# Kernel optimization log

Hardware: AMD Instinct MI355X
Metric: run time of the kernel (lower is better)

The kernel has to match this reference:

```python
import jax, jax.numpy as jnp
import numpy as np

N = 100000   # nodes
E = 1600000  # edges (avg degree 16)
D = 64       # in_dim == emb_dim
L = 3        # num_layers
G = 2000     # graphs in batch
LN_EPS = 1e-5


def setup_inputs() -> dict:
    key = jax.random.key(0)
    ks = jax.random.split(key, 14)
    s = 0.05  # xavier-ish small init scale
    x = jax.random.normal(ks[0], (N, D), jnp.float32)
    edge_index = jax.random.randint(ks[1], (2, E), 0, N, dtype=jnp.int32)
    batch = jnp.sort(jax.random.randint(ks[2], (N,), 0, G, dtype=jnp.int32))
    return {
        "x": x,
        "edge_index": edge_index,
        "batch": batch,
        # stacked per-layer GIN MLP params: Linear(D,D) -> SiLU -> Linear(D,D)
        "W1": jax.random.normal(ks[3], (L, D, D), jnp.float32) * s,
        "b1": jnp.zeros((L, D), jnp.float32),
        "W2": jax.random.normal(ks[4], (L, D, D), jnp.float32) * s,
        "b2": jnp.zeros((L, D), jnp.float32),
        "eps": jnp.zeros((L,), jnp.float32),  # trainable eps, init 0
        "ln_g": jnp.ones((L, D), jnp.float32),
        "ln_b": jnp.zeros((L, D), jnp.float32),
        # gate_nn: Linear(D, D//2) -> SiLU -> Linear(D//2, 1)
        "gw1": jax.random.normal(ks[5], (D, D // 2), jnp.float32) * s,
        "gb1": jnp.zeros((D // 2,), jnp.float32),
        "gw2": jax.random.normal(ks[6], (D // 2, 1), jnp.float32) * s,
        "gb2": jnp.zeros((1,), jnp.float32),
    }


def _layernorm(h, g, b):
    mu = jnp.mean(h, axis=-1, keepdims=True)
    var = jnp.mean(jnp.square(h - mu), axis=-1, keepdims=True)
    return (h - mu) * jax.lax.rsqrt(var + LN_EPS) * g + b


def reference(x, edge_index, batch, W1, b1, W2, b2, eps, ln_g, ln_b, gw1, gb1, gw2, gb2):
    src, dst = edge_index[0], edge_index[1]
    # ---- GIN layers (eval mode: dropout is identity) ----
    for l in range(L):
        agg = jax.ops.segment_sum(x[src], dst, num_segments=N)  # scatter-add of neighbor feats
        h = (1.0 + eps[l]) * x + agg                             # GIN update
        h = jax.nn.silu(h @ W1[l] + b1[l]) @ W2[l] + b2[l]       # 2-layer MLP
        x = _layernorm(h, ln_g[l], ln_b[l])
    # ---- GlobalAttention pooling ----
    gate = (jax.nn.silu(x @ gw1 + gb1) @ gw2 + gb2)[:, 0]        # [N]
    m = jax.ops.segment_max(gate, batch, num_segments=G)         # per-graph max for stability
    e = jnp.exp(gate - m[batch])
    denom = jax.ops.segment_sum(e, batch, num_segments=G)
    a = e / denom[batch]                                         # per-graph softmax
    out = jax.ops.segment_sum(a[:, None] * x, batch, num_segments=G)  # [G, D]
    return out
```

## Files before the change

kernel.cpp:

```cpp
#include <hip/hip_runtime.h>
#include <math.h>

#define NN 100000
#define NE 1600000
#define D 64
#define NG 2000
#define LN_EPS 1e-5f
#define NB ((NN + 255) / 256)
#define NBK NB
#define NTILE ((NN + 63) / 64)
#define EPB 6400
#define CAP 6144
#define LSTR 72
#define WFRAG_MLP 24576
#define WFRAG_TOT 26624
#define CONV_BLK ((NN * D) / 256)
#define WPREP_BLK (WFRAG_TOT / 256)

typedef __attribute__((ext_vector_type(8))) short short8;
typedef __attribute__((ext_vector_type(8))) unsigned short ushort8;
typedef __attribute__((ext_vector_type(4))) float floatx4;

__device__ __forceinline__ unsigned short f2bf(float f) {
    unsigned int u = __float_as_uint(f);
    u += 0x7FFF + ((u >> 16) & 1);
    return (unsigned short)(u >> 16);
}
__device__ __forceinline__ float bfu2f(unsigned short v) {
    return __uint_as_float(((unsigned int)v) << 16);
}

__global__ __launch_bounds__(256) void k_prep(const float* __restrict__ x,
                                              unsigned short* __restrict__ xb,
                                              const float* __restrict__ W1,
                                              const float* __restrict__ W2,
                                              const float* __restrict__ gw1,
                                              unsigned short* __restrict__ wfrag,
                                              int* __restrict__ bcur) {
    int b = blockIdx.x;
    int tid = threadIdx.x;
    if (b < CONV_BLK) {
        int i = b * 256 + tid;
        xb[i] = f2bf(x[i]);
    } else if (b < CONV_BLK + WPREP_BLK) {
        int idx = (b - CONV_BLK) * 256 + tid;
        if (idx < WFRAG_MLP) {
            int l = idx / 8192;
            int rem = idx % 8192;
            int mat = rem / 4096;
            int r2 = rem % 4096;
            int ks = r2 / 2048;
            int c = (r2 / 512) % 4;
            int lane = (r2 / 8) % 64;
            int j = r2 % 8;
            int n = lane & 15, q = lane >> 4;
            int k = ks * 32 + q * 8 + j;
            int col = c * 16 + n;
            const float* Wm = mat ? W2 : W1;
            wfrag[idx] = f2bf(Wm[l * 4096 + k * 64 + col]);
        } else {
            int g = idx - WFRAG_MLP;
            int ks = g / 1024;
            int c = (g / 512) % 2;
            int lane = (g / 8) % 64;
            int j = g % 8;
            int n = lane & 15, q = lane >> 4;
            int k = ks * 32 + q * 8 + j;
            wfrag[idx] = f2bf(gw1[k * 32 + c * 16 + n]);
        }
    } else {
        for (int i = tid; i < NBK; i += 256) bcur[i * 16] = i * CAP;
    }
}

__global__ __launch_bounds__(256) void k_part(const int* __restrict__ src,
                                              const int* __restrict__ dst,
                                              int* __restrict__ bcur,
                                              unsigned int* __restrict__ colbuf) {
    __shared__ int lcnt[NBK];
    __shared__ int lbase[NBK];
    __shared__ int sd[EPB];
    __shared__ int ss[EPB];
    int e0 = blockIdx.x * EPB;
    int tid = threadIdx.x;

    for (int i = tid; i < NBK; i += 256) lcnt[i] = 0;
    __syncthreads();

    for (int k = 0; k < EPB; k += 256) {
        int d = dst[e0 + k + tid];
        int s = src[e0 + k + tid];
        sd[k + tid] = d;
        ss[k + tid] = s;
        atomicAdd(&lcnt[d >> 8], 1);
    }
    __syncthreads();

    for (int i = tid; i < NBK; i += 256) {
        int c = lcnt[i];
        lbase[i] = c ? atomicAdd(&bcur[i * 16], c) : 0;
        lcnt[i] = 0;
    }
    __syncthreads();

    for (int k = 0; k < EPB; k += 256) {
        int d = sd[k + tid];
        int s = ss[k + tid];
        int b = d >> 8;
        int pos = lbase[b] + atomicAdd(&lcnt[b], 1);
        colbuf[pos] = ((unsigned int)s << 8) | (unsigned int)(d & 255);
    }
}

__global__ __launch_bounds__(256) void k_bfill(unsigned int* __restrict__ colbuf,
                                               const int* __restrict__ bcur,
                                               int* __restrict__ rps,
                                               int* __restrict__ rpe) {
    __shared__ unsigned int sld[CAP];
    __shared__ int lcur[256];
    __shared__ int wsum[4];
    int b = blockIdx.x;
    int ebase = b * CAP;
    int cnt = bcur[b * 16] - ebase;
    int nb0 = b * 256;
    int nodes = min(256, NN - nb0);
    int tid = threadIdx.x;
    int lane = tid & 63;
    int w = tid >> 6;

    for (int e = tid; e < cnt; e += 256) sld[e] = colbuf[ebase + e];
    lcur[tid] = 0;
    __syncthreads();

    for (int e = tid; e < cnt; e += 256)
        atomicAdd(&lcur[sld[e] & 255], 1);
    __syncthreads();

    int v = lcur[tid];
    int x = v;
#pragma unroll
    for (int off = 1; off < 64; off <<= 1) {
        int u = __shfl_up(x, off, 64);
        if (lane >= off) x += u;
    }
    if (lane == 63) wsum[w] = x;
    __syncthreads();
    int base = ebase;
    for (int k = 0; k < w; k++) base += wsum[k];
    int rp = base + x - v;
    if (tid < nodes) {
        rps[nb0 + tid] = rp;
        rpe[nb0 + tid] = rp + v;
    }
    lcur[tid] = rp;
    __syncthreads();

    for (int e = tid; e < cnt; e += 256) {
        unsigned int p = sld[e];
        int pos = atomicAdd(&lcur[p & 255], 1);
        colbuf[pos] = p >> 8;
    }
}

__global__ __launch_bounds__(256) void k_gather(const unsigned short* __restrict__ xin,
                                                unsigned short* __restrict__ h,
                                                const int* __restrict__ rps,
                                                const int* __restrict__ rpe,
                                                const int* __restrict__ col,
                                                const float* __restrict__ epsp) {
    int w = threadIdx.x >> 6;
    int lane = threadIdx.x & 63;
    int g = lane >> 3;
    int fl = lane & 7;
    int node = (blockIdx.x * 4 + w) * 8 + g;
    int start = rps[node], end = rpe[node];

    float a0 = 0.f, a1 = 0.f, a2 = 0.f, a3 = 0.f, a4 = 0.f, a5 = 0.f, a6 = 0.f, a7 = 0.f;
    int eb = start;
    for (; eb + 8 <= end; eb += 8) {
        int c = col[eb + fl];
        ushort8 v[8];
#pragma unroll
        for (int j = 0; j < 8; j++) {
            int idx = __shfl(c, g * 8 + j, 64);
            v[j] = *(const ushort8*)(xin + ((size_t)idx << 6) + fl * 8);
        }
#pragma unroll
        for (int j = 0; j < 8; j++) {
            a0 += bfu2f(v[j][0]); a1 += bfu2f(v[j][1]);
            a2 += bfu2f(v[j][2]); a3 += bfu2f(v[j][3]);
            a4 += bfu2f(v[j][4]); a5 += bfu2f(v[j][5]);
            a6 += bfu2f(v[j][6]); a7 += bfu2f(v[j][7]);
        }
    }
    if (eb < end) {
        int cnt = end - eb;
        int c = (fl < cnt) ? col[eb + fl] : 0;
        int j = 0;
        for (; j + 4 <= cnt; j += 4) {
            int i0 = __shfl(c, g * 8 + j, 64);
            int i1 = __shfl(c, g * 8 + j + 1, 64);
            int i2 = __shfl(c, g * 8 + j + 2, 64);
            int i3 = __shfl(c, g * 8 + j + 3, 64);
            ushort8 v0 = *(const ushort8*)(xin + ((size_t)i0 << 6) + fl * 8);
            ushort8 v1 = *(const ushort8*)(xin + ((size_t)i1 << 6) + fl * 8);
            ushort8 v2 = *(const ushort8*)(xin + ((size_t)i2 << 6) + fl * 8);
            ushort8 v3 = *(const ushort8*)(xin + ((size_t)i3 << 6) + fl * 8);
            a0 += bfu2f(v0[0]) + bfu2f(v1[0]) + bfu2f(v2[0]) + bfu2f(v3[0]);
            a1 += bfu2f(v0[1]) + bfu2f(v1[1]) + bfu2f(v2[1]) + bfu2f(v3[1]);
            a2 += bfu2f(v0[2]) + bfu2f(v1[2]) + bfu2f(v2[2]) + bfu2f(v3[2]);
            a3 += bfu2f(v0[3]) + bfu2f(v1[3]) + bfu2f(v2[3]) + bfu2f(v3[3]);
            a4 += bfu2f(v0[4]) + bfu2f(v1[4]) + bfu2f(v2[4]) + bfu2f(v3[4]);
            a5 += bfu2f(v0[5]) + bfu2f(v1[5]) + bfu2f(v2[5]) + bfu2f(v3[5]);
            a6 += bfu2f(v0[6]) + bfu2f(v1[6]) + bfu2f(v2[6]) + bfu2f(v3[6]);
            a7 += bfu2f(v0[7]) + bfu2f(v1[7]) + bfu2f(v2[7]) + bfu2f(v3[7]);
        }
        for (; j < cnt; j++) {
            int i0 = __shfl(c, g * 8 + j, 64);
            ushort8 v0 = *(const ushort8*)(xin + ((size_t)i0 << 6) + fl * 8);
            a0 += bfu2f(v0[0]); a1 += bfu2f(v0[1]);
            a2 += bfu2f(v0[2]); a3 += bfu2f(v0[3]);
            a4 += bfu2f(v0[4]); a5 += bfu2f(v0[5]);
            a6 += bfu2f(v0[6]); a7 += bfu2f(v0[7]);
        }
    }
    float ev = 1.0f + *epsp;
    ushort8 xs = *(const ushort8*)(xin + ((size_t)node << 6) + fl * 8);
    ushort8 o;
    o[0] = f2bf(ev * bfu2f(xs[0]) + a0);
    o[1] = f2bf(ev * bfu2f(xs[1]) + a1);
    o[2] = f2bf(ev * bfu2f(xs[2]) + a2);
    o[3] = f2bf(ev * bfu2f(xs[3]) + a3);
    o[4] = f2bf(ev * bfu2f(xs[4]) + a4);
    o[5] = f2bf(ev * bfu2f(xs[5]) + a5);
    o[6] = f2bf(ev * bfu2f(xs[6]) + a6);
    o[7] = f2bf(ev * bfu2f(xs[7]) + a7);
    *(ushort8*)(h + ((size_t)node << 6) + fl * 8) = o;
}

template <int LAST>
__global__ __launch_bounds__(256) void k_mfma(const unsigned short* __restrict__ h,
                                              unsigned short* __restrict__ xout,
                                              const short8* __restrict__ wf,
                                              const short8* __restrict__ gf,
                                              const float* __restrict__ b1,
                                              const float* __restrict__ b2,
                                              const float* __restrict__ lng,
                                              const float* __restrict__ lnb,
                                              const float* __restrict__ gb1,
                                              const float* __restrict__ gw2,
                                              const float* __restrict__ gb2,
                                              float* __restrict__ gate) {
    __shared__ __align__(16) unsigned short a2[4][16 * LSTR];
    int w = threadIdx.x >> 6;
    int lane = threadIdx.x & 63;
    int n = lane & 15;
    int q = lane >> 4;
    int base = blockIdx.x * 64 + w * 16;

    short8 B1f[2][4], B2f[2][4];
#pragma unroll
    for (int ks = 0; ks < 2; ks++)
#pragma unroll
        for (int c = 0; c < 4; c++) {
            B1f[ks][c] = wf[(ks * 4 + c) * 64 + lane];
            B2f[ks][c] = wf[512 + (ks * 4 + c) * 64 + lane];
        }
    short8 B3f[2][2];
    if (LAST) {
#pragma unroll
        for (int ks = 0; ks < 2; ks++)
#pragma unroll
            for (int c = 0; c < 2; c++)
                B3f[ks][c] = gf[(ks * 2 + c) * 64 + lane];
    }

    float b1v[4], b2v[4], lgv[4], lbv[4];
#pragma unroll
    for (int c = 0; c < 4; c++) {
        b1v[c] = b1[c * 16 + n];
        b2v[c] = b2[c * 16 + n];
        lgv[c] = lng[c * 16 + n];
        lbv[c] = lnb[c * 16 + n];
    }
    float gb1v[2], gw2v[2], gb2v = 0.f;
    if (LAST) {
        gb1v[0] = gb1[n]; gb1v[1] = gb1[16 + n];
        gw2v[0] = gw2[n]; gw2v[1] = gw2[16 + n];
        gb2v = gb2[0];
    }

    unsigned short* aw = a2[w];

    int mnode = base + n;
    int mc = min(mnode, NN - 1);
    const short8* hp = (const short8*)(h + ((size_t)mc << 6));
    short8 A0 = hp[q];
    short8 A1 = hp[4 + q];

    floatx4 acc1[4];
#pragma unroll
    for (int c = 0; c < 4; c++) {
        floatx4 a = {b1v[c], b1v[c], b1v[c], b1v[c]};
        a = __builtin_amdgcn_mfma_f32_16x16x32_bf16(A0, B1f[0][c], a, 0, 0, 0);
        a = __builtin_amdgcn_mfma_f32_16x16x32_bf16(A1, B1f[1][c], a, 0, 0, 0);
        acc1[c] = a;
    }

#pragma unroll
    for (int c = 0; c < 4; c++)
#pragma unroll
        for (int r = 0; r < 4; r++) {
            float v = acc1[c][r];
            v = v / (1.0f + __expf(-v));
            aw[(q * 4 + r) * LSTR + c * 16 + n] = f2bf(v);
        }

    const short8* ap = (const short8*)(aw + n * LSTR);
    short8 A20 = ap[q];
    short8 A21 = ap[4 + q];

    floatx4 acc2[4];
#pragma unroll
    for (int c = 0; c < 4; c++) {
        floatx4 a = {b2v[c], b2v[c], b2v[c], b2v[c]};
        a = __builtin_amdgcn_mfma_f32_16x16x32_bf16(A20, B2f[0][c], a, 0, 0, 0);
        a = __builtin_amdgcn_mfma_f32_16x16x32_bf16(A21, B2f[1][c], a, 0, 0, 0);
        acc2[c] = a;
    }

    float mu[4], inv[4];
#pragma unroll
    for (int r = 0; r < 4; r++) {
        float s = acc2[0][r] + acc2[1][r] + acc2[2][r] + acc2[3][r];
#pragma unroll
        for (int off = 1; off < 16; off <<= 1) s += __shfl_xor(s, off, 64);
        mu[r] = s * (1.0f / 64.0f);
        float d0 = acc2[0][r] - mu[r], d1 = acc2[1][r] - mu[r];
        float d2 = acc2[2][r] - mu[r], d3 = acc2[3][r] - mu[r];
        float vv = d0 * d0 + d1 * d1 + d2 * d2 + d3 * d3;
#pragma unroll
        for (int off = 1; off < 16; off <<= 1) vv += __shfl_xor(vv, off, 64);
        inv[r] = rsqrtf(vv * (1.0f / 64.0f) + LN_EPS);
    }

#pragma unroll
    for (int c = 0; c < 4; c++)
#pragma unroll
        for (int r = 0; r < 4; r++) {
            int node = base + q * 4 + r;
            float o = (acc2[c][r] - mu[r]) * inv[r] * lgv[c] + lbv[c];
            unsigned short ob = f2bf(o);
            if (node < NN) xout[((size_t)node << 6) + c * 16 + n] = ob;
            if (LAST) aw[(q * 4 + r) * LSTR + c * 16 + n] = ob;
        }

    if (LAST) {
        short8 G0 = ap[q];
        short8 G1 = ap[4 + q];
        floatx4 acc3[2];
#pragma unroll
        for (int c = 0; c < 2; c++) {
            floatx4 a = {gb1v[c], gb1v[c], gb1v[c], gb1v[c]};
            a = __builtin_amdgcn_mfma_f32_16x16x32_bf16(G0, B3f[0][c], a, 0, 0, 0);
            a = __builtin_amdgcn_mfma_f32_16x16x32_bf16(G1, B3f[1][c], a, 0, 0, 0);
            acc3[c] = a;
        }
#pragma unroll
        for (int r = 0; r < 4; r++) {
            float v0 = acc3[0][r];
            v0 = v0 / (1.0f + __expf(-v0));
            float v1 = acc3[1][r];
            v1 = v1 / (1.0f + __expf(-v1));
            float gsum = v0 * gw2v[0] + v1 * gw2v[1];
#pragma unroll
            for (int off = 1; off < 16; off <<= 1) gsum += __shfl_xor(gsum, off, 64);
            int node = base + q * 4 + r;
            if (n == 0 && node < NN) gate[node] = gsum + gb2v;
        }
    }
}

__global__ __launch_bounds__(256) void k_pool(const unsigned short* __restrict__ xf,
                                              const float* __restrict__ gate,
                                              const int* __restrict__ batch,
                                              float* __restrict__ out) {
    __shared__ float redm[4];
    __shared__ float reds[4];
    __shared__ float racc[4][D];
    int g = blockIdx.x;
    int w = threadIdx.x >> 6;
    int lane = threadIdx.x & 63;

    int lo = 0, hi = NN;
    while (lo < hi) { int mid = (lo + hi) >> 1; if (batch[mid] < g) lo = mid + 1; else hi = mid; }
    int start = lo;
    hi = NN;
    while (lo < hi) { int mid = (lo + hi) >> 1; if (batch[mid] < g + 1) lo = mid + 1; else hi = mid; }
    int end = lo;

    if (start >= end) {
        if (w == 0) out[((size_t)g << 6) + lane] = 0.0f;
        return;
    }

    float m = -INFINITY;
    for (int i = start + (int)threadIdx.x; i < end; i += 256) m = fmaxf(m, gate[i]);
#pragma unroll
    for (int mm = 32; mm >= 1; mm >>= 1) m = fmaxf(m, __shfl_xor(m, mm, 64));
    if (lane == 0) redm[w] = m;
    __syncthreads();
    m = fmaxf(fmaxf(redm[0], redm[1]), fmaxf(redm[2], redm[3]));

    float s = 0.0f;
    for (int i = start + (int)threadIdx.x; i < end; i += 256) s += __expf(gate[i] - m);
#pragma unroll
    for (int mm = 32; mm >= 1; mm >>= 1) s += __shfl_xor(s, mm, 64);
    if (lane == 0) reds[w] = s;
    __syncthreads();
    s = (reds[0] + reds[1]) + (reds[2] + reds[3]);

    float acc = 0.0f;
    for (int i = start + w; i < end; i += 4)
        acc += __expf(gate[i] - m) * bfu2f(xf[((size_t)i << 6) + lane]);
    racc[w][lane] = acc;
    __syncthreads();
    if (w == 0)
        out[((size_t)g << 6) + lane] =
            ((racc[0][lane] + racc[1][lane]) + (racc[2][lane] + racc[3][lane])) / s;
}

extern "C" void kernel_launch(void* const* d_in, const int* in_sizes, int n_in,
                              void* d_out, int out_size, void* d_ws, size_t ws_size,
                              hipStream_t stream) {
    const float* x   = (const float*)d_in[0];
    const int* ei    = (const int*)d_in[1];
    const int* batch = (const int*)d_in[2];
    const float* W1  = (const float*)d_in[3];
    const float* b1  = (const float*)d_in[4];
    const float* W2  = (const float*)d_in[5];
    const float* b2  = (const float*)d_in[6];
    const float* eps = (const float*)d_in[7];
    const float* lng = (const float*)d_in[8];
    const float* lnb = (const float*)d_in[9];
    const float* gw1 = (const float*)d_in[10];
    const float* gb1 = (const float*)d_in[11];
    const float* gw2 = (const float*)d_in[12];
    const float* gb2 = (const float*)d_in[13];

    const int* src = ei;
    const int* dst = ei + NE;

    unsigned short* xb    = (unsigned short*)d_ws;
    unsigned short* h     = xb + (size_t)NN * D;
    float* gate           = (float*)(h + (size_t)NN * D);
    int* rps              = (int*)(gate + NN);
    int* rpe              = rps + NN;
    int* colbuf           = rpe + NN;
    int* bcur             = colbuf + (size_t)NBK * CAP;
    unsigned short* wfrag = (unsigned short*)(bcur + NBK * 16);

    float* out = (float*)d_out;

    k_prep<<<CONV_BLK + WPREP_BLK + 1, 256, 0, stream>>>(x, xb, W1, W2, gw1, wfrag, bcur);
    k_part<<<NE / EPB, 256, 0, stream>>>(src, dst, bcur, (unsigned int*)colbuf);
    k_bfill<<<NBK, 256, 0, stream>>>((unsigned int*)colbuf, bcur, rps, rpe);

    const short8* wf0 = (const short8*)(wfrag);
    const short8* wf1 = (const short8*)(wfrag + 8192);
    const short8* wf2 = (const short8*)(wfrag + 16384);
    const short8* gf  = (const short8*)(wfrag + WFRAG_MLP);

    k_gather<<<NN / 32, 256, 0, stream>>>(xb, h, rps, rpe, colbuf, eps + 0);
    k_mfma<0><<<NTILE, 256, 0, stream>>>(h, xb, wf0, gf,
        b1 + 0 * D, b2 + 0 * D, lng + 0 * D, lnb + 0 * D, gb1, gw2, gb2, gate);

    k_gather<<<NN / 32, 256, 0, stream>>>(xb, h, rps, rpe, colbuf, eps + 1);
    k_mfma<0><<<NTILE, 256, 0, stream>>>(h, xb, wf1, gf,
        b1 + 1 * D, b2 + 1 * D, lng + 1 * D, lnb + 1 * D, gb1, gw2, gb2, gate);

    k_gather<<<NN / 32, 256, 0, stream>>>(xb, h, rps, rpe, colbuf, eps + 2);
    k_mfma<1><<<NTILE, 256, 0, stream>>>(h, xb, wf2, gf,
        b1 + 2 * D, b2 + 2 * D, lng + 2 * D, lnb + 2 * D, gb1, gw2, gb2, gate);

    k_pool<<<NG, 256, 0, stream>>>(xb, gate, batch, out);
}
```

Measured before the change: 297.5 us.

## Fuse edge partition into prep kernel and drop LDS staging in bucket fill

Merges the edge-partitioning pass into the input/weight conversion kernel, now run with 1024-thread blocks, which removes one kernel launch. The bucket cursor is zeroed with a memset and stores relative counts. The bucket-fill kernel no longer stages edges in shared memory; it reads colbuf from global memory twice and writes to a separate col array instead of in place. The self-feature load in gather moves ahead of the edge loop so its latency overlaps the neighbour loads. The costs are extra global reads in bucket fill, a second edge buffer, and partition blocks that now read dst twice from global memory instead of keeping it in LDS.

```diff
diff --git a/kernel.cpp b/kernel.cpp
--- a/kernel.cpp
+++ b/kernel.cpp
@@ -10,12 +10,13 @@
 #define NBK NB
 #define NTILE ((NN + 63) / 64)
 #define EPB 6400
+#define NPART (NE / EPB)
 #define CAP 6144
 #define LSTR 72
 #define WFRAG_MLP 24576
 #define WFRAG_TOT 26624
-#define CONV_BLK ((NN * D) / 256)
-#define WPREP_BLK (WFRAG_TOT / 256)
+#define CONV1K ((NN * D) / 1024)
+#define WPREP1K (WFRAG_TOT / 1024)
 
 typedef __attribute__((ext_vector_type(8))) short short8;
 typedef __attribute__((ext_vector_type(8))) unsigned short ushort8;
@@ -30,20 +31,49 @@
     return __uint_as_float(((unsigned int)v) << 16);
 }
 
-__global__ __launch_bounds__(256) void k_prep(const float* __restrict__ x,
-                                              unsigned short* __restrict__ xb,
-                                              const float* __restrict__ W1,
-                                              const float* __restrict__ W2,
-                                              const float* __restrict__ gw1,
-                                              unsigned short* __restrict__ wfrag,
-                                              int* __restrict__ bcur) {
+__global__ __launch_bounds__(1024) void k_prep_part(const float* __restrict__ x,
+                                                    unsigned short* __restrict__ xb,
+                                                    const float* __restrict__ W1,
+                                                    const float* __restrict__ W2,
+                                                    const float* __restrict__ gw1,
+                                                    unsigned short* __restrict__ wfrag,
+                                                    const int* __restrict__ src,
+                                                    const int* __restrict__ dst,
+                                                    int* __restrict__ bcur,
+                                                    unsigned int* __restrict__ colbuf) {
+    __shared__ int lcnt[NBK];
+    __shared__ int lbase[NBK];
     int b = blockIdx.x;
     int tid = threadIdx.x;
-    if (b < CONV_BLK) {
-        int i = b * 256 + tid;
+
+    if (b < NPART) {
+        int e0 = b * EPB;
+        for (int i = tid; i < NBK; i += 1024) lcnt[i] = 0;
+        __syncthreads();
+
+        for (int e = tid; e < EPB; e += 1024)
+            atomicAdd(&lcnt[dst[e0 + e] >> 8], 1);
+        __syncthreads();
+
+        for (int i = tid; i < NBK; i += 1024) {
+            int c = lcnt[i];
+            lbase[i] = c ? (i * CAP + atomicAdd(&bcur[i * 16], c)) : 0;
+            lcnt[i] = 0;
+        }
+        __syncthreads();
+
+        for (int e = tid; e < EPB; e += 1024) {
+            int d = dst[e0 + e];
+            int s = src[e0 + e];
+            int bk = d >> 8;
+            int pos = lbase[bk] + atomicAdd(&lcnt[bk], 1);
+            colbuf[pos] = ((unsigned int)s << 8) | (unsigned int)(d & 255);
+        }
+    } else if (b < NPART + CONV1K) {
+        int i = (b - NPART) * 1024 + tid;
         xb[i] = f2bf(x[i]);
-    } else if (b < CONV_BLK + WPREP_BLK) {
-        int idx = (b - CONV_BLK) * 256 + tid;
+    } else {
+        int idx = (b - NPART - CONV1K) * 1024 + tid;
         if (idx < WFRAG_MLP) {
             int l = idx / 8192;
             int rem = idx % 8192;
@@ -68,72 +98,30 @@
             int k = ks * 32 + q * 8 + j;
             wfrag[idx] = f2bf(gw1[k * 32 + c * 16 + n]);
         }
-    } else {
-        for (int i = tid; i < NBK; i += 256) bcur[i * 16] = i * CAP;
-    }
-}
-
-__global__ __launch_bounds__(256) void k_part(const int* __restrict__ src,
-                                              const int* __restrict__ dst,
-                                              int* __restrict__ bcur,
-                                              unsigned int* __restrict__ colbuf) {
-    __shared__ int lcnt[NBK];
-    __shared__ int lbase[NBK];
-    __shared__ int sd[EPB];
-    __shared__ int ss[EPB];
-    int e0 = blockIdx.x * EPB;
-    int tid = threadIdx.x;
-
-    for (int i = tid; i < NBK; i += 256) lcnt[i] = 0;
-    __syncthreads();
-
-    for (int k = 0; k < EPB; k += 256) {
-        int d = dst[e0 + k + tid];
-        int s = src[e0 + k + tid];
-        sd[k + tid] = d;
-        ss[k + tid] = s;
-        atomicAdd(&lcnt[d >> 8], 1);
-    }
-    __syncthreads();
-
-    for (int i = tid; i < NBK; i += 256) {
-        int c = lcnt[i];
-        lbase[i] = c ? atomicAdd(&bcur[i * 16], c) : 0;
-        lcnt[i] = 0;
-    }
-    __syncthreads();
-
-    for (int k = 0; k < EPB; k += 256) {
-        int d = sd[k + tid];
-        int s = ss[k + tid];
-        int b = d >> 8;
-        int pos = lbase[b] + atomicAdd(&lcnt[b], 1);
-        colbuf[pos] = ((unsigned int)s << 8) | (unsigned int)(d & 255);
-    }
-}
-
-__global__ __launch_bounds__(256) void k_bfill(unsigned int* __restrict__ colbuf,
+    }
+}
+
+__global__ __launch_bounds__(256) void k_bfill(const unsigned int* __restrict__ colbuf,
                                                const int* __restrict__ bcur,
                                                int* __restrict__ rps,
-                                               int* __restrict__ rpe) {
-    __shared__ unsigned int sld[CAP];
+                                               int* __restrict__ rpe,
+                                               int* __restrict__ col) {
     __shared__ int lcur[256];
     __shared__ int wsum[4];
     int b = blockIdx.x;
     int ebase = b * CAP;
-    int cnt = bcur[b * 16] - ebase;
+    int cnt = bcur[b * 16];
     int nb0 = b * 256;
     int nodes = min(256, NN - nb0);
     int tid = threadIdx.x;
     int lane = tid & 63;
     int w = tid >> 6;
 
-    for (int e = tid; e < cnt; e += 256) sld[e] = colbuf[ebase + e];
     lcur[tid] = 0;
     __syncthreads();
 
     for (int e = tid; e < cnt; e += 256)
-        atomicAdd(&lcur[sld[e] & 255], 1);
+        atomicAdd(&lcur[colbuf[ebase + e] & 255], 1);
     __syncthreads();
 
     int v = lcur[tid];
@@ -156,9 +144,9 @@
     __syncthreads();
 
     for (int e = tid; e < cnt; e += 256) {
-        unsigned int p = sld[e];
+        unsigned int p = colbuf[ebase + e];
         int pos = atomicAdd(&lcur[p & 255], 1);
-        colbuf[pos] = p >> 8;
+        col[pos] = p >> 8;
     }
 }
 
@@ -174,6 +162,8 @@
     int fl = lane & 7;
     int node = (blockIdx.x * 4 + w) * 8 + g;
     int start = rps[node], end = rpe[node];
+
+    ushort8 xs = *(const ushort8*)(xin + ((size_t)node << 6) + fl * 8);
 
     float a0 = 0.f, a1 = 0.f, a2 = 0.f, a3 = 0.f, a4 = 0.f, a5 = 0.f, a6 = 0.f, a7 = 0.f;
     int eb = start;
@@ -225,7 +215,6 @@
         }
     }
     float ev = 1.0f + *epsp;
-    ushort8 xs = *(const ushort8*)(xin + ((size_t)node << 6) + fl * 8);
     ushort8 o;
     o[0] = f2bf(ev * bfu2f(xs[0]) + a0);
     o[1] = f2bf(ev * bfu2f(xs[1]) + a1);
@@ -457,29 +446,31 @@
     int* rps              = (int*)(gate + NN);
     int* rpe              = rps + NN;
     int* colbuf           = rpe + NN;
-    int* bcur             = colbuf + (size_t)NBK * CAP;
+    int* col              = colbuf + (size_t)NBK * CAP;
+    int* bcur             = col + (size_t)NBK * CAP;
     unsigned short* wfrag = (unsigned short*)(bcur + NBK * 16);
 
     float* out = (float*)d_out;
 
-    k_prep<<<CONV_BLK + WPREP_BLK + 1, 256, 0, stream>>>(x, xb, W1, W2, gw1, wfrag, bcur);
-    k_part<<<NE / EPB, 256, 0, stream>>>(src, dst, bcur, (unsigned int*)colbuf);
-    k_bfill<<<NBK, 256, 0, stream>>>((unsigned int*)colbuf, bcur, rps, rpe);
+    hipMemsetAsync(bcur, 0, NBK * 16 * sizeof(int), stream);
+    k_prep_part<<<NPART + CONV1K + WPREP1K, 1024, 0, stream>>>(
+        x, xb, W1, W2, gw1, wfrag, src, dst, bcur, (unsigned int*)colbuf);
+    k_bfill<<<NBK, 256, 0, stream>>>((unsigned int*)colbuf, bcur, rps, rpe, col);
 
     const short8* wf0 = (const short8*)(wfrag);
     const short8* wf1 = (const short8*)(wfrag + 8192);
     const short8* wf2 = (const short8*)(wfrag + 16384);
     const short8* gf  = (const short8*)(wfrag + WFRAG_MLP);
 
-    k_gather<<<NN / 32, 256, 0, stream>>>(xb, h, rps, rpe, colbuf, eps + 0);
+    k_gather<<<NN / 32, 256, 0, stream>>>(xb, h, rps, rpe, col, eps + 0);
     k_mfma<0><<<NTILE, 256, 0, stream>>>(h, xb, wf0, gf,
         b1 + 0 * D, b2 + 0 * D, lng + 0 * D, lnb + 0 * D, gb1, gw2, gb2, gate);
 
-    k_gather<<<NN / 32, 256, 0, stream>>>(xb, h, rps, rpe, colbuf, eps + 1);
+    k_gather<<<NN / 32, 256, 0, stream>>>(xb, h, rps, rpe, col, eps + 1);
     k_mfma<0><<<NTILE, 256, 0, stream>>>(h, xb, wf1, gf,
         b1 + 1 * D, b2 + 1 * D, lng + 1 * D, lnb + 1 * D, gb1, gw2, gb2, gate);
 
-    k_gather<<<NN / 32, 256, 0, stream>>>(xb, h, rps, rpe, colbuf, eps + 2);
+    k_gather<<<NN / 32, 256, 0, stream>>>(xb, h, rps, rpe, col, eps + 2);
     k_mfma<1><<<NTILE, 256, 0, stream>>>(h, xb, wf2, gf,
         b1 + 2 * D, b2 + 2 * D, lng + 2 * D, lnb + 2 * D, gb1, gw2, gb2, gate);
 
```

New measurement: 292.6 us. No clear change (-1.6%).
